# Kernel tuning notes

Hardware: AMD Instinct MI355X
Metric: run time of the kernel (lower is better)

## Reference

```python
import jax, jax.numpy as jnp
import numpy as np

EPS = 1e-5  # BatchNorm eps (PyTorch default)


def gcn_conv(x, edge_index, W, b):
    """PyG GCNConv with add_self_loops=True, normalize=True.
    out[j] = sum_{(i->j)} x_w[i] / sqrt(deg_i * deg_j) + x_w[j] / deg_j + b,
    deg_j = 1 + in-degree(j) (self-loop included)."""
    n = x.shape[0]
    src, dst = edge_index[0], edge_index[1]
    ones = jnp.ones(src.shape[0], x.dtype)
    deg = 1.0 + jax.ops.segment_sum(ones, dst, num_segments=n)  # [n]
    dis = jax.lax.rsqrt(deg)
    xw = x @ W  # [n, out]
    msg = xw[src] * (dis[src] * dis[dst])[:, None]  # gather + per-edge norm
    agg = jax.ops.segment_sum(msg, dst, num_segments=n)  # scatter-add
    agg = agg + xw * (1.0 / deg)[:, None]  # self-loop term
    return agg + b


def bn_relu(x, gamma, beta):
    # BatchNorm1d over the node dim (training-mode batch stats) + ReLU
    mean = x.mean(axis=0)
    var = x.var(axis=0)
    return jax.nn.relu((x - mean) * jax.lax.rsqrt(var + EPS) * gamma + beta)


def wireframe_gnn(x, edge_index, layers, fcW, fcb):
    feats = [x]
    h = x
    for (W, b, g, be) in layers:  # fixed small n_layers loop
        h = bn_relu(gcn_conv(h, edge_index, W, b), g, be)
        feats.append(h)
    cat = jnp.concatenate(feats, axis=1)
    return jax.nn.relu(cat @ fcW + fcb)


N_L, N_J = 50000, 25000
D_FC, NF = 1024, 256
E_L, E_J = 400000, 100000
L_LAB, J_LAB = 10, 3


def setup_inputs() -> dict:
    key = jax.random.key(0)
    ks = iter(jax.random.split(key, 48))
    p = lambda shape: (jax.random.normal(next(ks), shape, jnp.float32) * 0.02)
    inp = {}
    inp["line_features"] = jax.random.normal(next(ks), (N_L, D_FC), jnp.float32)
    inp["junction_features"] = jax.random.normal(next(ks), (N_J, NF), jnp.float32)
    inp["line_edge_index"] = jax.random.randint(next(ks), (2, E_L), 0, N_L, jnp.int64)
    inp["junction_edge_index"] = jax.random.randint(next(ks), (2, E_J), 0, N_J, jnp.int64)
    # line GNN: 1024 -> 512 -> 256, concat 1792 -> fc 1024
    inp["lg_W1"], inp["lg_b1"] = p((D_FC, D_FC // 2)), p((D_FC // 2,))
    inp["lg_g1"], inp["lg_be1"] = jnp.ones(D_FC // 2, jnp.float32), jnp.zeros(D_FC // 2, jnp.float32)
    inp["lg_W2"], inp["lg_b2"] = p((D_FC // 2, D_FC // 4)), p((D_FC // 4,))
    inp["lg_g2"], inp["lg_be2"] = jnp.ones(D_FC // 4, jnp.float32), jnp.zeros(D_FC // 4, jnp.float32)
    cat_l = D_FC + D_FC // 2 + D_FC // 4  # 1792
    inp["lg_fcW"], inp["lg_fcb"] = p((cat_l, D_FC)), p((D_FC,))
    # fc_lines: 1024 -> 1024 -> 1024 -> L_LAB (dim_loi*n_pts1 == dim_fc == 1024)
    inp["fl_W1"], inp["fl_b1"] = p((D_FC, D_FC)), p((D_FC,))
    inp["fl_W2"], inp["fl_b2"] = p((D_FC, D_FC)), p((D_FC,))
    inp["fl_W3"], inp["fl_b3"] = p((D_FC, L_LAB)), p((L_LAB,))
    # junction GNN: 256 -> 128 -> 64, concat 448 -> fc 256
    inp["jg_W1"], inp["jg_b1"] = p((NF, NF // 2)), p((NF // 2,))
    inp["jg_g1"], inp["jg_be1"] = jnp.ones(NF // 2, jnp.float32), jnp.zeros(NF // 2, jnp.float32)
    inp["jg_W2"], inp["jg_b2"] = p((NF // 2, NF // 4)), p((NF // 4,))
    inp["jg_g2"], inp["jg_be2"] = jnp.ones(NF // 4, jnp.float32), jnp.zeros(NF // 4, jnp.float32)
    cat_j = NF + NF // 2 + NF // 4  # 448
    inp["jg_fcW"], inp["jg_fcb"] = p((cat_j, NF)), p((NF,))
    # fc_junction: 256 -> 64 -> J_LAB
    m = NF // 4
    inp["fj_W1"], inp["fj_b1"] = p((NF, m)), p((m,))
    inp["fj_W2"], inp["fj_b2"] = p((m, J_LAB)), p((J_LAB,))
    return inp


def reference(line_features, junction_features, line_edge_index, junction_edge_index,
              lg_W1, lg_b1, lg_g1, lg_be1, lg_W2, lg_b2, lg_g2, lg_be2, lg_fcW, lg_fcb,
              fl_W1, fl_b1, fl_W2, fl_b2, fl_W3, fl_b3,
              jg_W1, jg_b1, jg_g1, jg_be1, jg_W2, jg_b2, jg_g2, jg_be2, jg_fcW, jg_fcb,
              fj_W1, fj_b1, fj_W2, fj_b2):
    # line branch
    h = wireframe_gnn(line_features, line_edge_index,
                      [(lg_W1, lg_b1, lg_g1, lg_be1), (lg_W2, lg_b2, lg_g2, lg_be2)],
                      lg_fcW, lg_fcb)
    h = jax.nn.relu(h @ fl_W1 + fl_b1)
    h = jax.nn.relu(h @ fl_W2 + fl_b2)
    line_logits = h @ fl_W3 + fl_b3
    # junction branch
    g = wireframe_gnn(junction_features, junction_edge_index,
                      [(jg_W1, jg_b1, jg_g1, jg_be1), (jg_W2, jg_b2, jg_g2, jg_be2)],
                      jg_fcW, jg_fcb)
    g = jax.nn.relu(g @ fj_W1 + fj_b1)
    junction_logits = g @ fj_W2 + fj_b2
    return (line_logits, junction_logits)
```

## Files before the change

kernel.cpp:

```cpp
#include <hip/hip_runtime.h>
#include <stdint.h>
#include <stddef.h>

typedef _Float16 f16;
typedef _Float16 f16x8 __attribute__((ext_vector_type(8)));
typedef _Float16 f16x4_t __attribute__((ext_vector_type(4)));
typedef float floatx4 __attribute__((ext_vector_type(4)));

template <int N> struct F16Vec { typedef f16 type __attribute__((ext_vector_type(N))); };

#define BN_EPS 1e-5f

struct WtJob { const float* W; f16* Wt; int K; int N; int base; };
struct WtBatch { WtJob j[12]; int njobs; int total; };

__global__ void k_wt_all(WtBatch b) {
  int t = blockIdx.x * blockDim.x + threadIdx.x;
  if (t >= b.total) return;
  int i = 0;
  #pragma unroll 1
  while (i + 1 < b.njobs && t >= b.j[i + 1].base) ++i;
  WtJob J = b.j[i];
  int r = t - J.base;
  int k = r / J.N, n = r - k * J.N;
  J.Wt[(size_t)n * J.K + k] = (f16)J.W[r];
}

__global__ void k_cvt_cols(const float* __restrict__ src, f16* __restrict__ dst,
                           int n, int c, int ldd, int coff) {
  int t = blockIdx.x * blockDim.x + threadIdx.x;
  int cq = c >> 2;
  if (t >= n * cq) return;
  int r = t / cq, j = (t - r * cq) << 2;
  float4 v = *(const float4*)(src + (size_t)r * c + j);
  f16x4_t o; o[0] = (f16)v.x; o[1] = (f16)v.y; o[2] = (f16)v.z; o[3] = (f16)v.w;
  *(f16x4_t*)(dst + (size_t)r * ldd + coff + j) = o;
}

__global__ void k_count(const int* __restrict__ dst, int E, int* __restrict__ cnt) {
  int t = blockIdx.x * blockDim.x + threadIdx.x;
  if (t < E) atomicAdd(&cnt[dst[t]], 1);
}

__global__ void k_scan(const int* __restrict__ cnt, int n, int* __restrict__ rowstart,
                       float* __restrict__ dis) {
  __shared__ int wsum[16];
  __shared__ int carry_s;
  int tid = threadIdx.x, lane = tid & 63, wv = tid >> 6;
  if (tid == 0) { carry_s = 0; rowstart[0] = 0; }
  __syncthreads();
  for (int base = 0; base < n; base += 1024) {
    int i = base + tid;
    int x = (i < n) ? cnt[i] : 0;
    int orig = x;
    #pragma unroll
    for (int off = 1; off < 64; off <<= 1) {
      int y = __shfl_up(x, off, 64);
      if (lane >= off) x += y;
    }
    if (lane == 63) wsum[wv] = x;
    __syncthreads();
    if (wv == 0) {
      int s = (lane < 16) ? wsum[lane] : 0;
      #pragma unroll
      for (int off = 1; off < 16; off <<= 1) {
        int y = __shfl_up(s, off, 64);
        if (lane >= off) s += y;
      }
      if (lane < 16) wsum[lane] = s;
    }
    __syncthreads();
    int waveoff = (wv == 0) ? 0 : wsum[wv - 1];
    int incl = x + waveoff + carry_s;
    if (i < n) {
      rowstart[i + 1] = incl;
      dis[i] = rsqrtf(1.0f + (float)orig);
    }
    __syncthreads();
    if (tid == 1023) carry_s = incl;
    __syncthreads();
  }
}

__global__ void k_fill(const int* __restrict__ ei, int E, const int* __restrict__ rowstart,
                       int* __restrict__ fill, int* __restrict__ colidx) {
  int t = blockIdx.x * blockDim.x + threadIdx.x;
  if (t >= E) return;
  int s = ei[t], d = ei[E + t];
  int pos = atomicAdd(&fill[d], 1);
  colidx[rowstart[d] + pos] = s;
}

template <int CPL>
__global__ void k_gather_v(const f16* __restrict__ xw, int C,
                           const int* __restrict__ rowstart, const int* __restrict__ colidx,
                           const float* __restrict__ dis, const float* __restrict__ bias,
                           float* __restrict__ vbuf, int n) {
  typedef typename F16Vec<CPL>::type V;
  int w = threadIdx.x >> 6, l = threadIdx.x & 63;
  int j = blockIdx.x * 4 + w;
  if (j >= n) return;
  float dj = dis[j];
  int rs = rowstart[j], re = rowstart[j + 1];
  int c0 = l * CPL;
  float acc[CPL];
  {
    V p = *(const V*)(xw + (size_t)j * C + c0);
    float s = dj * dj;
    #pragma unroll
    for (int t = 0; t < CPL; ++t) acc[t] = (float)p[t] * s;
  }
  int e = rs;
  for (; e + 2 <= re; e += 2) {
    int s0 = colidx[e], s1 = colidx[e + 1];
    float f0 = dis[s0] * dj, f1 = dis[s1] * dj;
    V p0 = *(const V*)(xw + (size_t)s0 * C + c0);
    V p1 = *(const V*)(xw + (size_t)s1 * C + c0);
    #pragma unroll
    for (int t = 0; t < CPL; ++t) acc[t] += (float)p0[t] * f0 + (float)p1[t] * f1;
  }
  if (e < re) {
    int s0 = colidx[e];
    float f0 = dis[s0] * dj;
    V p0 = *(const V*)(xw + (size_t)s0 * C + c0);
    #pragma unroll
    for (int t = 0; t < CPL; ++t) acc[t] += (float)p0[t] * f0;
  }
  float* o = vbuf + (size_t)j * C + c0;
  #pragma unroll
  for (int t = 0; t < CPL; ++t) o[t] = acc[t] + bias[c0 + t];
}

__global__ void k_stats(const float* __restrict__ v, int n, int C,
                        float* __restrict__ sum, float* __restrict__ sumsq) {
  int c = blockIdx.x * blockDim.x + threadIdx.x;
  if (c >= C) return;
  int r0 = blockIdx.y * 128, r1 = min(r0 + 128, n);
  float s = 0.f, s2 = 0.f;
  for (int r = r0; r < r1; ++r) {
    float x = v[(size_t)r * C + c];
    s += x; s2 += x * x;
  }
  atomicAdd(&sum[c], s);
  atomicAdd(&sumsq[c], s2);
}

__global__ void k_bnparam(const float* __restrict__ sum, const float* __restrict__ sumsq,
                          const float* __restrict__ gamma, const float* __restrict__ beta,
                          int n, int C, float* __restrict__ scale, float* __restrict__ shift) {
  int c = blockIdx.x * blockDim.x + threadIdx.x;
  if (c >= C) return;
  float mean = sum[c] / (float)n;
  float var = sumsq[c] / (float)n - mean * mean;
  float sc = gamma[c] * rsqrtf(var + BN_EPS);
  scale[c] = sc;
  shift[c] = beta[c] - mean * sc;
}

__global__ void k_bnapply(const float* __restrict__ v, int n, int C,
                          const float* __restrict__ scale, const float* __restrict__ shift,
                          f16* __restrict__ dst, int ldd, int coff) {
  int t = blockIdx.x * blockDim.x + threadIdx.x;
  int cq = C >> 2;
  if (t >= n * cq) return;
  int r = t / cq, c = (t - r * cq) << 2;
  float4 x = *(const float4*)(v + (size_t)r * C + c);
  float4 sc = *(const float4*)(scale + c);
  float4 sh = *(const float4*)(shift + c);
  f16x4_t o;
  o[0] = (f16)fmaxf(x.x * sc.x + sh.x, 0.f);
  o[1] = (f16)fmaxf(x.y * sc.y + sh.y, 0.f);
  o[2] = (f16)fmaxf(x.z * sc.z + sh.z, 0.f);
  o[3] = (f16)fmaxf(x.w * sc.w + sh.w, 0.f);
  *(f16x4_t*)(dst + (size_t)r * ldd + coff + c) = o;
}

__global__ __launch_bounds__(256)
void k_gemm(const f16* __restrict__ A, int lda,
            const f16* __restrict__ Bt,
            void* __restrict__ Cv, int ldc,
            const float* __restrict__ bias, int relu, int outf,
            int M, int N, int K, int mt, int nt, int per) {
  __shared__ f16 Ash[128 * 64];
  __shared__ f16 Bsh[128 * 64];
  int b = blockIdx.x;
  int g = (b & 7) * per + (b >> 3);
  if (g >= mt * nt) return;
  int tm = (g / nt) * 128, tn = (g % nt) * 128;

  int tid = threadIdx.x;
  int l = tid & 63, w = tid >> 6;

  const f16* ag[4]; const f16* bg[4];
  uint32_t lof[4];
  #pragma unroll
  for (int j = 0; j < 4; ++j) {
    int rl = w * 32 + j * 8 + (l >> 3);
    int ck = l & 7;
    int lc = ck ^ (rl & 7);
    int gr = tm + rl; if (gr > M - 1) gr = M - 1;
    int gn = tn + rl; if (gn > N - 1) gn = N - 1;
    ag[j] = A + (size_t)gr * lda + lc * 8;
    bg[j] = Bt + (size_t)gn * K + lc * 8;
    lof[j] = (uint32_t)(w * 32 + j * 8) * 128;
  }

  int wm = (w >> 1) * 64, wn = (w & 1) * 64;
  int q = l >> 4, l15 = l & 15;
  const f16x8* apf[4][2]; const f16x8* bpf[4][2];
  #pragma unroll
  for (int i = 0; i < 4; ++i) {
    int m = wm + i * 16 + l15;
    int n2 = wn + i * 16 + l15;
    #pragma unroll
    for (int kk = 0; kk < 2; ++kk) {
      apf[i][kk] = (const f16x8*)&Ash[m * 64 + (((kk << 2) | q) ^ (m & 7)) * 8];
      bpf[i][kk] = (const f16x8*)&Bsh[n2 * 64 + (((kk << 2) | q) ^ (n2 & 7)) * 8];
    }
  }

  floatx4 acc[4][4];
  #pragma unroll
  for (int i = 0; i < 4; ++i)
    #pragma unroll
    for (int j = 0; j < 4; ++j) acc[i][j] = (floatx4){0.f, 0.f, 0.f, 0.f};

  for (int k0 = 0; k0 < K; k0 += 64) {
    if (k0) __syncthreads();
    #pragma unroll
    for (int j = 0; j < 4; ++j) {
      __builtin_amdgcn_global_load_lds(
          (const __attribute__((address_space(1))) void*)ag[j],
          (__attribute__((address_space(3))) void*)((char*)Ash + lof[j]), 16, 0, 0);
      __builtin_amdgcn_global_load_lds(
          (const __attribute__((address_space(1))) void*)bg[j],
          (__attribute__((address_space(3))) void*)((char*)Bsh + lof[j]), 16, 0, 0);
      ag[j] += 64; bg[j] += 64;
    }
    __syncthreads();
    #pragma unroll
    for (int kk = 0; kk < 2; ++kk) {
      f16x8 af[4], bf[4];
      #pragma unroll
      for (int i = 0; i < 4; ++i) { af[i] = *apf[i][kk]; bf[i] = *bpf[i][kk]; }
      #pragma unroll
      for (int mi = 0; mi < 4; ++mi)
        #pragma unroll
        for (int ni = 0; ni < 4; ++ni)
          acc[mi][ni] = __builtin_amdgcn_mfma_f32_16x16x32_f16(af[mi], bf[ni], acc[mi][ni], 0, 0, 0);
    }
  }

  #pragma unroll
  for (int ni = 0; ni < 4; ++ni) {
    int col = tn + wn + ni * 16 + l15;
    if (col >= N) continue;
    float bv = bias ? bias[col] : 0.f;
    #pragma unroll
    for (int mi = 0; mi < 4; ++mi) {
      int rowb = tm + wm + mi * 16 + q * 4;
      #pragma unroll
      for (int r = 0; r < 4; ++r) {
        int row = rowb + r;
        if (row < M) {
          float v = acc[mi][ni][r] + bv;
          if (relu) v = fmaxf(v, 0.f);
          if (outf) ((float*)Cv)[(size_t)row * ldc + col] = v;
          else      ((f16*)Cv)[(size_t)row * ldc + col] = (f16)v;
        }
      }
    }
  }
}

extern "C" void kernel_launch(void* const* d_in, const int* in_sizes, int n_in,
                              void* d_out, int out_size, void* d_ws, size_t ws_size,
                              hipStream_t stream) {
  (void)in_sizes; (void)n_in; (void)out_size; (void)ws_size;
  const int NL = 50000, NJ = 25000, EL = 400000, EJ = 100000;

  const float* x_l  = (const float*)d_in[0];
  const float* x_j  = (const float*)d_in[1];
  const int*   ei_l = (const int*)d_in[2];
  const int*   ei_j = (const int*)d_in[3];
  const float* lgW1 = (const float*)d_in[4];  const float* lgb1 = (const float*)d_in[5];
  const float* lgg1 = (const float*)d_in[6];  const float* lgbe1= (const float*)d_in[7];
  const float* lgW2 = (const float*)d_in[8];  const float* lgb2 = (const float*)d_in[9];
  const float* lgg2 = (const float*)d_in[10]; const float* lgbe2= (const float*)d_in[11];
  const float* lgfcW= (const float*)d_in[12]; const float* lgfcb= (const float*)d_in[13];
  const float* flW1 = (const float*)d_in[14]; const float* flb1 = (const float*)d_in[15];
  const float* flW2 = (const float*)d_in[16]; const float* flb2 = (const float*)d_in[17];
  const float* flW3 = (const float*)d_in[18]; const float* flb3 = (const float*)d_in[19];
  const float* jgW1 = (const float*)d_in[20]; const float* jgb1 = (const float*)d_in[21];
  const float* jgg1 = (const float*)d_in[22]; const float* jgbe1= (const float*)d_in[23];
  const float* jgW2 = (const float*)d_in[24]; const float* jgb2 = (const float*)d_in[25];
  const float* jgg2 = (const float*)d_in[26]; const float* jgbe2= (const float*)d_in[27];
  const float* jgfcW= (const float*)d_in[28]; const float* jgfcb= (const float*)d_in[29];
  const float* fjW1 = (const float*)d_in[30]; const float* fjb1 = (const float*)d_in[31];
  const float* fjW2 = (const float*)d_in[32]; const float* fjb2 = (const float*)d_in[33];

  char* ws = (char*)d_ws;
  size_t off = 0;
  auto alloc = [&](size_t bytes) -> char* {
    char* p = ws + off;
    off += (bytes + 255) & ~(size_t)255;
    return p;
  };

  f16* cat16 = (f16*)alloc((size_t)NL * 1792 * 2);
  f16* hA    = (f16*)alloc((size_t)NL * 1024 * 2);
  f16* hB    = (f16*)alloc((size_t)NL * 1024 * 2);
  float* vbuf = (float*)hA;
  f16*  xw16  = (f16*)hB;
  f16* catJ  = (f16*)alloc((size_t)NJ * 448 * 2);
  f16* hJA   = (f16*)alloc((size_t)NJ * 256 * 2);
  f16* hJB   = (f16*)alloc((size_t)NJ * 64 * 2);
  float* vbufJ = (float*)hA;
  f16*  xwJ   = (f16*)hB;

  f16* W1t   = (f16*)alloc((size_t)1024 * 512 * 2);
  f16* W2t   = (f16*)alloc((size_t)512 * 256 * 2);
  f16* fcWt  = (f16*)alloc((size_t)1792 * 1024 * 2);
  f16* flW1t = (f16*)alloc((size_t)1024 * 1024 * 2);
  f16* flW2t = (f16*)alloc((size_t)1024 * 1024 * 2);
  f16* flW3t = (f16*)alloc((size_t)1024 * 16 * 2);
  f16* jW1t  = (f16*)alloc((size_t)256 * 128 * 2);
  f16* jW2t  = (f16*)alloc((size_t)128 * 64 * 2);
  f16* jfcWt = (f16*)alloc((size_t)448 * 256 * 2);
  f16* fjW1t = (f16*)alloc((size_t)256 * 64 * 2);
  f16* fjW2t = (f16*)alloc((size_t)64 * 4 * 2);

  int* cntL  = (int*)alloc((size_t)2 * NL * 4);
  int* fillL = cntL + NL;
  int* rsL   = (int*)alloc((size_t)(NL + 1) * 4);
  int* cixL  = (int*)alloc((size_t)EL * 4);
  float* disL= (float*)alloc((size_t)NL * 4);
  int* cntJ  = (int*)alloc((size_t)2 * NJ * 4);
  int* fillJ = cntJ + NJ;
  int* rsJ   = (int*)alloc((size_t)(NJ + 1) * 4);
  int* cixJ  = (int*)alloc((size_t)EJ * 4);
  float* disJ= (float*)alloc((size_t)NJ * 4);
  float* sumc  = (float*)alloc(2 * 512 * 4);
  float* sumqc = sumc + 512;
  float* scalc = (float*)alloc(512 * 4);
  float* shftc = (float*)alloc(512 * 4);

  auto cdiv = [](int a, int b) { return (a + b - 1) / b; };

  auto gemm = [&](const f16* A, int lda, const f16* Bt, void* Cc, int ldc,
                  const float* bias, int relu, int outf, int M, int N, int K) {
    int mt = cdiv(M, 128), nt = cdiv(N, 128);
    int per = cdiv(mt * nt, 8);
    k_gemm<<<8 * per, 256, 0, stream>>>(A, lda, Bt, Cc, ldc, bias, relu, outf,
                                        M, N, K, mt, nt, per);
  };
  auto csr = [&](const int* ei, int E, int n, int* cnt, int* rs, int* fill,
                 int* cix, float* dis) {
    hipMemsetAsync(cnt, 0, (size_t)2 * n * 4, stream);
    k_count<<<cdiv(E, 256), 256, 0, stream>>>(ei + E, E, cnt);
    k_scan<<<1, 1024, 0, stream>>>(cnt, n, rs, dis);
    k_fill<<<cdiv(E, 256), 256, 0, stream>>>(ei, E, rs, fill, cix);
  };
  auto bn = [&](float* v, int n, int C, const float* gamma, const float* beta,
                f16* dst, int ldd, int coff) {
    hipMemsetAsync(sumc, 0, (size_t)2 * 512 * 4, stream);
    dim3 gs(cdiv(C, 256), cdiv(n, 128));
    k_stats<<<gs, 256, 0, stream>>>(v, n, C, sumc, sumqc);
    k_bnparam<<<cdiv(C, 256), 256, 0, stream>>>(sumc, sumqc, gamma, beta, n, C, scalc, shftc);
    k_bnapply<<<cdiv(n * (C >> 2), 256), 256, 0, stream>>>(v, n, C, scalc, shftc, dst, ldd, coff);
  };

  {
    WtBatch B2; int base = 0, nj = 0;
    auto add = [&](const float* W, f16* Wt, int K, int N) {
      B2.j[nj++] = WtJob{W, Wt, K, N, base};
      base += K * N;
    };
    add(lgW1, W1t, 1024, 512);
    add(lgW2, W2t, 512, 256);
    add(lgfcW, fcWt, 1792, 1024);
    add(flW1, flW1t, 1024, 1024);
    add(flW2, flW2t, 1024, 1024);
    add(flW3, flW3t, 1024, 10);
    add(jgW1, jW1t, 256, 128);
    add(jgW2, jW2t, 128, 64);
    add(jgfcW, jfcWt, 448, 256);
    add(fjW1, fjW1t, 256, 64);
    add(fjW2, fjW2t, 64, 3);
    B2.njobs = nj; B2.total = base;
    k_wt_all<<<cdiv(base, 256), 256, 0, stream>>>(B2);
  }

  k_cvt_cols<<<cdiv(NL * 256, 256), 256, 0, stream>>>(x_l, cat16, NL, 1024, 1792, 0);
  k_cvt_cols<<<cdiv(NJ * 64, 256), 256, 0, stream>>>(x_j, catJ, NJ, 256, 448, 0);

  csr(ei_l, EL, NL, cntL, rsL, fillL, cixL, disL);

  gemm(cat16, 1792, W1t, xw16, 512, nullptr, 0, 0, NL, 512, 1024);
  k_gather_v<8><<<cdiv(NL, 4), 256, 0, stream>>>(xw16, 512, rsL, cixL, disL, lgb1, vbuf, NL);
  bn(vbuf, NL, 512, lgg1, lgbe1, cat16, 1792, 1024);

  gemm(cat16 + 1024, 1792, W2t, xw16, 256, nullptr, 0, 0, NL, 256, 512);
  k_gather_v<4><<<cdiv(NL, 4), 256, 0, stream>>>(xw16, 256, rsL, cixL, disL, lgb2, vbuf, NL);
  bn(vbuf, NL, 256, lgg2, lgbe2, cat16, 1792, 1536);

  gemm(cat16, 1792, fcWt, hA, 1024, lgfcb, 1, 0, NL, 1024, 1792);
  gemm(hA, 1024, flW1t, hB, 1024, flb1, 1, 0, NL, 1024, 1024);
  gemm(hB, 1024, flW2t, hA, 1024, flb2, 1, 0, NL, 1024, 1024);
  gemm(hA, 1024, flW3t, (float*)d_out, 10, flb3, 0, 1, NL, 10, 1024);

  csr(ei_j, EJ, NJ, cntJ, rsJ, fillJ, cixJ, disJ);

  gemm(catJ, 448, jW1t, xwJ, 128, nullptr, 0, 0, NJ, 128, 256);
  k_gather_v<2><<<cdiv(NJ, 4), 256, 0, stream>>>(xwJ, 128, rsJ, cixJ, disJ, jgb1, vbufJ, NJ);
  bn(vbufJ, NJ, 128, jgg1, jgbe1, catJ, 448, 256);

  gemm(catJ + 256, 448, jW2t, xwJ, 64, nullptr, 0, 0, NJ, 64, 128);
  k_gather_v<1><<<cdiv(NJ, 4), 256, 0, stream>>>(xwJ, 64, rsJ, cixJ, disJ, jgb2, vbufJ, NJ);
  bn(vbufJ, NJ, 64, jgg2, jgbe2, catJ, 448, 384);

  gemm(catJ, 448, jfcWt, hJA, 256, jgfcb, 1, 0, NJ, 256, 448);
  gemm(hJA, 256, fjW1t, hJB, 64, fjb1, 1, 0, NJ, 64, 256);
  gemm(hJB, 64, fjW2t, (float*)d_out + (size_t)NL * 10, 3, fjb2, 0, 1, NJ, 3, 64);
}
```

Before: 1.749 ms.

## Double-buffer GEMM K-loop, fuse CSR builds, keep GCN outputs in fp16

```diff
diff --git a/kernel.cpp b/kernel.cpp
--- a/kernel.cpp
+++ b/kernel.cpp
@@ -11,19 +11,30 @@
 
 #define BN_EPS 1e-5f
 
-struct WtJob { const float* W; f16* Wt; int K; int N; int base; };
-struct WtBatch { WtJob j[12]; int njobs; int total; };
-
-__global__ void k_wt_all(WtBatch b) {
-  int t = blockIdx.x * blockDim.x + threadIdx.x;
-  if (t >= b.total) return;
+struct WtJob { const float* W; f16* Wt; int K; int N; int tN; int tilebase; };
+struct WtBatch { WtJob j[12]; int njobs; int ntiles; };
+
+__global__ void k_wt_tiled(WtBatch b) {
+  __shared__ float T[32][33];
+  int bt = blockIdx.x;
   int i = 0;
   #pragma unroll 1
-  while (i + 1 < b.njobs && t >= b.j[i + 1].base) ++i;
+  while (i + 1 < b.njobs && bt >= b.j[i + 1].tilebase) ++i;
   WtJob J = b.j[i];
-  int r = t - J.base;
-  int k = r / J.N, n = r - k * J.N;
-  J.Wt[(size_t)n * J.K + k] = (f16)J.W[r];
+  int t = bt - J.tilebase;
+  int tr = t / J.tN, tc = t - tr * J.tN;
+  int ty = threadIdx.x >> 5, tx = threadIdx.x & 31;
+  #pragma unroll
+  for (int s = 0; s < 32; s += 8) {
+    int k = tr * 32 + ty + s, n = tc * 32 + tx;
+    if (k < J.K && n < J.N) T[ty + s][tx] = J.W[(size_t)k * J.N + n];
+  }
+  __syncthreads();
+  #pragma unroll
+  for (int s = 0; s < 32; s += 8) {
+    int n = tc * 32 + ty + s, k = tr * 32 + tx;
+    if (n < J.N && k < J.K) J.Wt[(size_t)n * J.K + k] = (f16)T[tx][ty + s];
+  }
 }
 
 __global__ void k_cvt_cols(const float* __restrict__ src, f16* __restrict__ dst,
@@ -37,22 +48,26 @@
   *(f16x4_t*)(dst + (size_t)r * ldd + coff + j) = o;
 }
 
-__global__ void k_count(const int* __restrict__ dst, int E, int* __restrict__ cnt) {
+__global__ void k_count2(const int* __restrict__ dL, int EL, int* __restrict__ cntL,
+                         const int* __restrict__ dJ, int EJ, int* __restrict__ cntJ) {
   int t = blockIdx.x * blockDim.x + threadIdx.x;
-  if (t < E) atomicAdd(&cnt[dst[t]], 1);
-}
-
-__global__ void k_scan(const int* __restrict__ cnt, int n, int* __restrict__ rowstart,
-                       float* __restrict__ dis) {
+  if (t < EL) atomicAdd(&cntL[dL[t]], 1);
+  else if (t < EL + EJ) atomicAdd(&cntJ[dJ[t - EL]], 1);
+}
+
+__global__ void k_scan4(const int* __restrict__ cnt, int n, int* __restrict__ rowstart,
+                        float* __restrict__ dis) {
   __shared__ int wsum[16];
   __shared__ int carry_s;
   int tid = threadIdx.x, lane = tid & 63, wv = tid >> 6;
   if (tid == 0) { carry_s = 0; rowstart[0] = 0; }
   __syncthreads();
-  for (int base = 0; base < n; base += 1024) {
-    int i = base + tid;
-    int x = (i < n) ? cnt[i] : 0;
-    int orig = x;
+  for (int base = 0; base < n; base += 4096) {
+    int i4 = base + tid * 4;
+    int4 c = {0, 0, 0, 0};
+    if (i4 < n) c = *(const int4*)(cnt + i4);
+    int s0 = c.x, s1 = s0 + c.y, s2 = s1 + c.z, s3 = s2 + c.w;
+    int x = s3;
     #pragma unroll
     for (int off = 1; off < 64; off <<= 1) {
       int y = __shfl_up(x, off, 64);
@@ -71,31 +86,45 @@
     }
     __syncthreads();
     int waveoff = (wv == 0) ? 0 : wsum[wv - 1];
-    int incl = x + waveoff + carry_s;
-    if (i < n) {
-      rowstart[i + 1] = incl;
-      dis[i] = rsqrtf(1.0f + (float)orig);
+    int excl = (x - s3) + waveoff + carry_s;
+    if (i4 < n) {
+      rowstart[i4 + 1] = excl + s0;
+      rowstart[i4 + 2] = excl + s1;
+      rowstart[i4 + 3] = excl + s2;
+      rowstart[i4 + 4] = excl + s3;
+      dis[i4 + 0] = rsqrtf(1.0f + (float)c.x);
+      dis[i4 + 1] = rsqrtf(1.0f + (float)c.y);
+      dis[i4 + 2] = rsqrtf(1.0f + (float)c.z);
+      dis[i4 + 3] = rsqrtf(1.0f + (float)c.w);
     }
     __syncthreads();
-    if (tid == 1023) carry_s = incl;
+    if (tid == 1023) carry_s = excl + s3;
     __syncthreads();
   }
 }
 
-__global__ void k_fill(const int* __restrict__ ei, int E, const int* __restrict__ rowstart,
-                       int* __restrict__ fill, int* __restrict__ colidx) {
+__global__ void k_fill2(const int* __restrict__ eiL, int EL, const int* __restrict__ rsL,
+                        int* __restrict__ fillL, int* __restrict__ cixL,
+                        const int* __restrict__ eiJ, int EJ, const int* __restrict__ rsJ,
+                        int* __restrict__ fillJ, int* __restrict__ cixJ) {
   int t = blockIdx.x * blockDim.x + threadIdx.x;
-  if (t >= E) return;
-  int s = ei[t], d = ei[E + t];
-  int pos = atomicAdd(&fill[d], 1);
-  colidx[rowstart[d] + pos] = s;
+  if (t < EL) {
+    int s = eiL[t], d = eiL[EL + t];
+    int pos = atomicAdd(&fillL[d], 1);
+    cixL[rsL[d] + pos] = s;
+  } else if (t < EL + EJ) {
+    int u = t - EL;
+    int s = eiJ[u], d = eiJ[EJ + u];
+    int pos = atomicAdd(&fillJ[d], 1);
+    cixJ[rsJ[d] + pos] = s;
+  }
 }
 
 template <int CPL>
-__global__ void k_gather_v(const f16* __restrict__ xw, int C,
-                           const int* __restrict__ rowstart, const int* __restrict__ colidx,
-                           const float* __restrict__ dis, const float* __restrict__ bias,
-                           float* __restrict__ vbuf, int n) {
+__global__ void k_gather_f16(const f16* __restrict__ xw, int C,
+                             const int* __restrict__ rowstart, const int* __restrict__ colidx,
+                             const float* __restrict__ dis, const float* __restrict__ bias,
+                             f16* __restrict__ dst, int ldd, int coff, int n) {
   typedef typename F16Vec<CPL>::type V;
   int w = threadIdx.x >> 6, l = threadIdx.x & 63;
   int j = blockIdx.x * 4 + w;
@@ -126,19 +155,20 @@
     #pragma unroll
     for (int t = 0; t < CPL; ++t) acc[t] += (float)p0[t] * f0;
   }
-  float* o = vbuf + (size_t)j * C + c0;
-  #pragma unroll
-  for (int t = 0; t < CPL; ++t) o[t] = acc[t] + bias[c0 + t];
-}
-
-__global__ void k_stats(const float* __restrict__ v, int n, int C,
+  V o;
+  #pragma unroll
+  for (int t = 0; t < CPL; ++t) o[t] = (f16)(acc[t] + bias[c0 + t]);
+  *(V*)(dst + (size_t)j * ldd + coff + c0) = o;
+}
+
+__global__ void k_stats(const f16* __restrict__ v, int ldd, int coff, int n, int C,
                         float* __restrict__ sum, float* __restrict__ sumsq) {
   int c = blockIdx.x * blockDim.x + threadIdx.x;
   if (c >= C) return;
   int r0 = blockIdx.y * 128, r1 = min(r0 + 128, n);
   float s = 0.f, s2 = 0.f;
   for (int r = r0; r < r1; ++r) {
-    float x = v[(size_t)r * C + c];
+    float x = (float)v[(size_t)r * ldd + coff + c];
     s += x; s2 += x * x;
   }
   atomicAdd(&sum[c], s);
@@ -157,22 +187,22 @@
   shift[c] = beta[c] - mean * sc;
 }
 
-__global__ void k_bnapply(const float* __restrict__ v, int n, int C,
-                          const float* __restrict__ scale, const float* __restrict__ shift,
-                          f16* __restrict__ dst, int ldd, int coff) {
+__global__ void k_bnapply_ip(f16* __restrict__ v, int ldd, int coff, int n, int C,
+                             const float* __restrict__ scale, const float* __restrict__ shift) {
   int t = blockIdx.x * blockDim.x + threadIdx.x;
   int cq = C >> 2;
   if (t >= n * cq) return;
   int r = t / cq, c = (t - r * cq) << 2;
-  float4 x = *(const float4*)(v + (size_t)r * C + c);
+  f16* p = v + (size_t)r * ldd + coff + c;
+  f16x4_t x = *(f16x4_t*)p;
   float4 sc = *(const float4*)(scale + c);
   float4 sh = *(const float4*)(shift + c);
   f16x4_t o;
-  o[0] = (f16)fmaxf(x.x * sc.x + sh.x, 0.f);
-  o[1] = (f16)fmaxf(x.y * sc.y + sh.y, 0.f);
-  o[2] = (f16)fmaxf(x.z * sc.z + sh.z, 0.f);
-  o[3] = (f16)fmaxf(x.w * sc.w + sh.w, 0.f);
-  *(f16x4_t*)(dst + (size_t)r * ldd + coff + c) = o;
+  o[0] = (f16)fmaxf((float)x[0] * sc.x + sh.x, 0.f);
+  o[1] = (f16)fmaxf((float)x[1] * sc.y + sh.y, 0.f);
+  o[2] = (f16)fmaxf((float)x[2] * sc.z + sh.z, 0.f);
+  o[3] = (f16)fmaxf((float)x[3] * sc.w + sh.w, 0.f);
+  *(f16x4_t*)p = o;
 }
 
 __global__ __launch_bounds__(256)
@@ -181,42 +211,37 @@
             void* __restrict__ Cv, int ldc,
             const float* __restrict__ bias, int relu, int outf,
             int M, int N, int K, int mt, int nt, int per) {
-  __shared__ f16 Ash[128 * 64];
-  __shared__ f16 Bsh[128 * 64];
+  __shared__ f16 Ash[2][128 * 32];
+  __shared__ f16 Bsh[2][128 * 32];
   int b = blockIdx.x;
   int g = (b & 7) * per + (b >> 3);
   if (g >= mt * nt) return;
   int tm = (g / nt) * 128, tn = (g % nt) * 128;
-
-  int tid = threadIdx.x;
-  int l = tid & 63, w = tid >> 6;
-
-  const f16* ag[4]; const f16* bg[4];
-  uint32_t lof[4];
-  #pragma unroll
-  for (int j = 0; j < 4; ++j) {
-    int rl = w * 32 + j * 8 + (l >> 3);
-    int ck = l & 7;
-    int lc = ck ^ (rl & 7);
+  int tid = threadIdx.x, l = tid & 63, w = tid >> 6;
+
+  const f16* ag[2]; const f16* bg[2];
+  uint32_t lof[2];
+  #pragma unroll
+  for (int j = 0; j < 2; ++j) {
+    int rl = w * 32 + j * 16 + (l >> 2);
+    int ck = l & 3;
+    int lc = ck ^ ((rl >> 1) & 3);
     int gr = tm + rl; if (gr > M - 1) gr = M - 1;
     int gn = tn + rl; if (gn > N - 1) gn = N - 1;
     ag[j] = A + (size_t)gr * lda + lc * 8;
     bg[j] = Bt + (size_t)gn * K + lc * 8;
-    lof[j] = (uint32_t)(w * 32 + j * 8) * 128;
+    lof[j] = (uint32_t)(w * 32 + j * 16) * 64;
   }
 
   int wm = (w >> 1) * 64, wn = (w & 1) * 64;
   int q = l >> 4, l15 = l & 15;
-  const f16x8* apf[4][2]; const f16x8* bpf[4][2];
+  uint32_t aoffb[4], boffb[4];
   #pragma unroll
   for (int i = 0; i < 4; ++i) {
     int m = wm + i * 16 + l15;
     int n2 = wn + i * 16 + l15;
-    #pragma unroll
-    for (int kk = 0; kk < 2; ++kk) {
-      apf[i][kk] = (const f16x8*)&Ash[m * 64 + (((kk << 2) | q) ^ (m & 7)) * 8];
-      bpf[i][kk] = (const f16x8*)&Bsh[n2 * 64 + (((kk << 2) | q) ^ (n2 & 7)) * 8];
-    }
+    aoffb[i] = (uint32_t)(m * 32 + (q ^ ((m >> 1) & 3)) * 8) * 2;
+    boffb[i] = (uint32_t)(n2 * 32 + (q ^ ((n2 >> 1) & 3)) * 8) * 2;
   }
 
   floatx4 acc[4][4];
@@ -225,30 +250,45 @@
     #pragma unroll
     for (int j = 0; j < 4; ++j) acc[i][j] = (floatx4){0.f, 0.f, 0.f, 0.f};
 
-  for (int k0 = 0; k0 < K; k0 += 64) {
-    if (k0) __syncthreads();
-    #pragma unroll
-    for (int j = 0; j < 4; ++j) {
-      __builtin_amdgcn_global_load_lds(
-          (const __attribute__((address_space(1))) void*)ag[j],
-          (__attribute__((address_space(3))) void*)((char*)Ash + lof[j]), 16, 0, 0);
-      __builtin_amdgcn_global_load_lds(
-          (const __attribute__((address_space(1))) void*)bg[j],
-          (__attribute__((address_space(3))) void*)((char*)Bsh + lof[j]), 16, 0, 0);
-      ag[j] += 64; bg[j] += 64;
-    }
+  int nk = K >> 5;
+  #pragma unroll
+  for (int j = 0; j < 2; ++j) {
+    __builtin_amdgcn_global_load_lds(
+        (const __attribute__((address_space(1))) void*)ag[j],
+        (__attribute__((address_space(3))) void*)((char*)Ash + lof[j]), 16, 0, 0);
+    __builtin_amdgcn_global_load_lds(
+        (const __attribute__((address_space(1))) void*)bg[j],
+        (__attribute__((address_space(3))) void*)((char*)Bsh + lof[j]), 16, 0, 0);
+    ag[j] += 32; bg[j] += 32;
+  }
+
+  for (int i = 0; i < nk; ++i) {
     __syncthreads();
-    #pragma unroll
-    for (int kk = 0; kk < 2; ++kk) {
-      f16x8 af[4], bf[4];
+    if (i + 1 < nk) {
+      uint32_t d = ((i + 1) & 1) ? 8192u : 0u;
       #pragma unroll
-      for (int i = 0; i < 4; ++i) { af[i] = *apf[i][kk]; bf[i] = *bpf[i][kk]; }
+      for (int j = 0; j < 2; ++j) {
+        __builtin_amdgcn_global_load_lds(
+            (const __attribute__((address_space(1))) void*)ag[j],
+            (__attribute__((address_space(3))) void*)((char*)Ash + d + lof[j]), 16, 0, 0);
+        __builtin_amdgcn_global_load_lds(
+            (const __attribute__((address_space(1))) void*)bg[j],
+            (__attribute__((address_space(3))) void*)((char*)Bsh + d + lof[j]), 16, 0, 0);
+        ag[j] += 32; bg[j] += 32;
+      }
+    }
+    uint32_t s = (i & 1) ? 8192u : 0u;
+    f16x8 af[4], bf[4];
+    #pragma unroll
+    for (int ii = 0; ii < 4; ++ii) {
+      af[ii] = *(const f16x8*)((const char*)Ash + s + aoffb[ii]);
+      bf[ii] = *(const f16x8*)((const char*)Bsh + s + boffb[ii]);
+    }
+    #pragma unroll
+    for (int mi = 0; mi < 4; ++mi)
       #pragma unroll
-      for (int mi = 0; mi < 4; ++mi)
-        #pragma unroll
-        for (int ni = 0; ni < 4; ++ni)
-          acc[mi][ni] = __builtin_amdgcn_mfma_f32_16x16x32_f16(af[mi], bf[ni], acc[mi][ni], 0, 0, 0);
-    }
+      for (int ni = 0; ni < 4; ++ni)
+        acc[mi][ni] = __builtin_amdgcn_mfma_f32_16x16x32_f16(af[mi], bf[ni], acc[mi][ni], 0, 0, 0);
   }
 
   #pragma unroll
@@ -310,12 +350,10 @@
   f16* cat16 = (f16*)alloc((size_t)NL * 1792 * 2);
   f16* hA    = (f16*)alloc((size_t)NL * 1024 * 2);
   f16* hB    = (f16*)alloc((size_t)NL * 1024 * 2);
-  float* vbuf = (float*)hA;
   f16*  xw16  = (f16*)hB;
   f16* catJ  = (f16*)alloc((size_t)NJ * 448 * 2);
   f16* hJA   = (f16*)alloc((size_t)NJ * 256 * 2);
   f16* hJB   = (f16*)alloc((size_t)NJ * 64 * 2);
-  float* vbufJ = (float*)hA;
   f16*  xwJ   = (f16*)hB;
 
   f16* W1t   = (f16*)alloc((size_t)1024 * 512 * 2);
@@ -330,18 +368,23 @@
   f16* fjW1t = (f16*)alloc((size_t)256 * 64 * 2);
   f16* fjW2t = (f16*)alloc((size_t)64 * 4 * 2);
 
-  int* cntL  = (int*)alloc((size_t)2 * NL * 4);
+  int* zero0 = (int*)alloc(((size_t)2 * NL + 2 * NJ + 1920) * 4);
+  int* cntL  = zero0;
   int* fillL = cntL + NL;
-  int* rsL   = (int*)alloc((size_t)(NL + 1) * 4);
+  int* cntJ  = fillL + NL;
+  int* fillJ = cntJ + NJ;
+  float* stats = (float*)(fillJ + NJ);
+  float* sum1L = stats;        float* sq1L = stats + 512;
+  float* sum2L = stats + 1024; float* sq2L = stats + 1280;
+  float* sum1J = stats + 1536; float* sq1J = stats + 1664;
+  float* sum2J = stats + 1792; float* sq2J = stats + 1856;
+
+  int* rsL   = (int*)alloc((size_t)(NL + 4) * 4);
   int* cixL  = (int*)alloc((size_t)EL * 4);
   float* disL= (float*)alloc((size_t)NL * 4);
-  int* cntJ  = (int*)alloc((size_t)2 * NJ * 4);
-  int* fillJ = cntJ + NJ;
-  int* rsJ   = (int*)alloc((size_t)(NJ + 1) * 4);
+  int* rsJ   = (int*)alloc((size_t)(NJ + 4) * 4);
   int* cixJ  = (int*)alloc((size_t)EJ * 4);
   float* disJ= (float*)alloc((size_t)NJ * 4);
-  float* sumc  = (float*)alloc(2 * 512 * 4);
-  float* sumqc = sumc + 512;
   float* scalc = (float*)alloc(512 * 4);
   float* shftc = (float*)alloc(512 * 4);
 
@@ -354,27 +397,22 @@
     k_gemm<<<8 * per, 256, 0, stream>>>(A, lda, Bt, Cc, ldc, bias, relu, outf,
                                         M, N, K, mt, nt, per);
   };
-  auto csr = [&](const int* ei, int E, int n, int* cnt, int* rs, int* fill,
-                 int* cix, float* dis) {
-    hipMemsetAsync(cnt, 0, (size_t)2 * n * 4, stream);
-    k_count<<<cdiv(E, 256), 256, 0, stream>>>(ei + E, E, cnt);
-    k_scan<<<1, 1024, 0, stream>>>(cnt, n, rs, dis);
-    k_fill<<<cdiv(E, 256), 256, 0, stream>>>(ei, E, rs, fill, cix);
+  auto bn = [&](f16* v, int ldd, int coff, int n, int C,
+                float* sum, float* sumsq, const float* gamma, const float* beta) {
+    dim3 gs(cdiv(C, 256), cdiv(n, 128));
+    k_stats<<<gs, 256, 0, stream>>>(v, ldd, coff, n, C, sum, sumsq);
+    k_bnparam<<<cdiv(C, 256), 256, 0, stream>>>(sum, sumsq, gamma, beta, n, C, scalc, shftc);
+    k_bnapply_ip<<<cdiv(n * (C >> 2), 256), 256, 0, stream>>>(v, ldd, coff, n, C, scalc, shftc);
   };
-  auto bn = [&](float* v, int n, int C, const float* gamma, const float* beta,
-                f16* dst, int ldd, int coff) {
-    hipMemsetAsync(sumc, 0, (size_t)2 * 512 * 4, stream);
-    dim3 gs(cdiv(C, 256), cdiv(n, 128));
-    k_stats<<<gs, 256, 0, stream>>>(v, n, C, sumc, sumqc);
-    k_bnparam<<<cdiv(C, 256), 256, 0, stream>>>(sumc, sumqc, gamma, beta, n, C, scalc, shftc);
-    k_bnapply<<<cdiv(n * (C >> 2), 256), 256, 0, stream>>>(v, n, C, scalc, shftc, dst, ldd, coff);
-  };
+
+  hipMemsetAsync(zero0, 0, ((size_t)2 * NL + 2 * NJ + 1920) * 4, stream);
 
   {
     WtBatch B2; int base = 0, nj = 0;
     auto add = [&](const float* W, f16* Wt, int K, int N) {
-      B2.j[nj++] = WtJob{W, Wt, K, N, base};
-      base += K * N;
+      int tK = cdiv(K, 32), tN = cdiv(N, 32);
+      B2.j[nj++] = WtJob{W, Wt, K, N, tN, base};
+      base += tK * tN;
     };
     add(lgW1, W1t, 1024, 512);
     add(lgW2, W2t, 512, 256);
@@ -387,37 +425,43 @@
     add(jgfcW, jfcWt, 448, 256);
     add(fjW1, fjW1t, 256, 64);
     add(fjW2, fjW2t, 64, 3);
-    B2.njobs = nj; B2.total = base;
-    k_wt_all<<<cdiv(base, 256), 256, 0, stream>>>(B2);
+    B2.njobs = nj; B2.ntiles = base;
+    k_wt_tiled<<<base, 256, 0, stream>>>(B2);
   }
 
   k_cvt_cols<<<cdiv(NL * 256, 256), 256, 0, stream>>>(x_l, cat16, NL, 1024, 1792, 0);
   k_cvt_cols<<<cdiv(NJ * 64, 256), 256, 0, stream>>>(x_j, catJ, NJ, 256, 448, 0);
 
-  csr(ei_l, EL, NL, cntL, rsL, fillL, cixL, disL);
+  k_count2<<<cdiv(EL + EJ, 256), 256, 0, stream>>>(ei_l + EL, EL, cntL, ei_j + EJ, EJ, cntJ);
+  k_scan4<<<1, 1024, 0, stream>>>(cntL, NL, rsL, disL);
+  k_scan4<<<1, 1024, 0, stream>>>(cntJ, NJ, rsJ, disJ);
+  k_fill2<<<cdiv(EL + EJ, 256), 256, 0, stream>>>(ei_l, EL, rsL, fillL, cixL,
+                                                  ei_j, EJ, rsJ, fillJ, cixJ);
 
   gemm(cat16, 1792, W1t, xw16, 512, nullptr, 0, 0, NL, 512, 1024);
-  k_gather_v<8><<<cdiv(NL, 4), 256, 0, stream>>>(xw16, 512, rsL, cixL, disL, lgb1, vbuf, NL);
-  bn(vbuf, NL, 512, lgg1, lgbe1, cat16, 1792, 1024);
+  k_gather_f16<8><<<cdiv(NL, 4), 256, 0, stream>>>(xw16, 512, rsL, cixL, disL, lgb1,
+                                                   cat16, 1792, 1024, NL);
+  bn(cat16, 1792, 1024, NL, 512, sum1L, sq1L, lgg1, lgbe1);
 
   gemm(cat16 + 1024, 1792, W2t, xw16, 256, nullptr, 0, 0, NL, 256, 512);
-  k_gather_v<4><<<cdiv(NL, 4), 256, 0, stream>>>(xw16, 256, rsL, cixL, disL, lgb2, vbuf, NL);
-  bn(vbuf, NL, 256, lgg2, lgbe2, cat16, 1792, 1536);
+  k_gather_f16<4><<<cdiv(NL, 4), 256, 0, stream>>>(xw16, 256, rsL, cixL, disL, lgb2,
+                                                   cat16, 1792, 1536, NL);
+  bn(cat16, 1792, 1536, NL, 256, sum2L, sq2L, lgg2, lgbe2);
 
   gemm(cat16, 1792, fcWt, hA, 1024, lgfcb, 1, 0, NL, 1024, 1792);
   gemm(hA, 1024, flW1t, hB, 1024, flb1, 1, 0, NL, 1024, 1024);
   gemm(hB, 1024, flW2t, hA, 1024, flb2, 1, 0, NL, 1024, 1024);
   gemm(hA, 1024, flW3t, (float*)d_out, 10, flb3, 0, 1, NL, 10, 1024);
 
-  csr(ei_j, EJ, NJ, cntJ, rsJ, fillJ, cixJ, disJ);
-
   gemm(catJ, 448, jW1t, xwJ, 128, nullptr, 0, 0, NJ, 128, 256);
-  k_gather_v<2><<<cdiv(NJ, 4), 256, 0, stream>>>(xwJ, 128, rsJ, cixJ, disJ, jgb1, vbufJ, NJ);
-  bn(vbufJ, NJ, 128, jgg1, jgbe1, catJ, 448, 256);
+  k_gather_f16<2><<<cdiv(NJ, 4), 256, 0, stream>>>(xwJ, 128, rsJ, cixJ, disJ, jgb1,
+                                                   catJ, 448, 256, NJ);
+  bn(catJ, 448, 256, NJ, 128, sum1J, sq1J, jgg1, jgbe1);
 
   gemm(catJ + 256, 448, jW2t, xwJ, 64, nullptr, 0, 0, NJ, 64, 128);
-  k_gather_v<1><<<cdiv(NJ, 4), 256, 0, stream>>>(xwJ, 64, rsJ, cixJ, disJ, jgb2, vbufJ, NJ);
-  bn(vbufJ, NJ, 64, jgg2, jgbe2, catJ, 448, 384);
+  k_gather_f16<1><<<cdiv(NJ, 4), 256, 0, stream>>>(xwJ, 64, rsJ, cixJ, disJ, jgb2,
+                                                   catJ, 448, 384, NJ);
+  bn(catJ, 448, 384, NJ, 64, sum2J, sq2J, jgg2, jgbe2);
 
   gemm(catJ, 448, jfcWt, hJA, 256, jgfcb, 1, 0, NJ, 256, 448);
   gemm(hJA, 256, fjW1t, hJB, 64, fjb1, 1, 0, NJ, 64, 256);
```

Result: no change. 1.727 ms (-1.3%).
